# Optimization experiments

Measured on AMD Instinct MI355X. Metric: run time of the kernel, lower is better.

The kernel has to match this reference:

```python
import math
import jax, jax.numpy as jnp
import numpy as np

B, T, C = 2, 2048, 1024
N_HEAD, N_KV_HEAD = 16, 4
HEAD_DIM = C // N_HEAD  # 64

def _rope(x, cos, sin):
    # x: (B, T, H, D); cos/sin: (1, T, 1, D//2)
    d = x.shape[3] // 2
    x1, x2 = x[..., :d], x[..., d:]
    return jnp.concatenate([x1 * cos + x2 * sin, -x1 * sin + x2 * cos], axis=3)

def _rms_norm(x):
    return x * jax.lax.rsqrt(jnp.mean(x * x, axis=-1, keepdims=True) + 1e-06)

def setup_inputs() -> dict:
    key = jax.random.key(0)
    ks = jax.random.split(key, 9)
    x = jax.random.normal(ks[0], (B, T, C), dtype=jnp.float32)
    ve = jax.random.normal(ks[1], (B, T, N_KV_HEAD * HEAD_DIM), dtype=jnp.float32)
    cos = jax.random.uniform(ks[2], (1, T, 1, HEAD_DIM // 2), dtype=jnp.float32)
    sin = jax.random.uniform(ks[3], (1, T, 1, HEAD_DIM // 2), dtype=jnp.float32)
    s = 1.0 / math.sqrt(C)
    Wq = jax.random.normal(ks[4], (C, N_HEAD * HEAD_DIM), dtype=jnp.float32) * s
    Wk = jax.random.normal(ks[5], (C, N_KV_HEAD * HEAD_DIM), dtype=jnp.float32) * s
    Wv = jax.random.normal(ks[6], (C, N_KV_HEAD * HEAD_DIM), dtype=jnp.float32) * s
    Wproj = jax.random.normal(ks[7], (C, C), dtype=jnp.float32) * s
    Wg = jax.random.normal(ks[8], (12, N_KV_HEAD), dtype=jnp.float32) * (1.0 / math.sqrt(12))
    return {"x": x, "ve": ve, "cos": cos, "sin": sin,
            "Wq": Wq, "Wk": Wk, "Wv": Wv, "Wproj": Wproj, "Wg": Wg,
            "window_size": 1024}

def reference(x, ve, cos, sin, Wq, Wk, Wv, Wproj, Wg, window_size):
    Bb, Tt, Cc = x.shape
    q = (x @ Wq).reshape(Bb, Tt, N_HEAD, HEAD_DIM)
    k = (x @ Wk).reshape(Bb, Tt, N_KV_HEAD, HEAD_DIM)
    v = (x @ Wv).reshape(Bb, Tt, N_KV_HEAD, HEAD_DIM)
    # value-embedding gate (has_ve layer)
    vee = ve.reshape(Bb, Tt, N_KV_HEAD, HEAD_DIM)
    gate = 3.0 * jax.nn.sigmoid(x[..., :12] @ Wg)  # (B, T, n_kv_head)
    v = v + gate[..., None] * vee
    q = _rope(q, cos, sin)
    k = _rope(k, cos, sin)
    q = _rms_norm(q) * 1.2
    k = _rms_norm(k) * 1.2
    repeats = N_HEAD // N_KV_HEAD
    k = jnp.repeat(k, repeats, axis=2)
    v = jnp.repeat(v, repeats, axis=2)
    # sliding-window causal mask
    row = jnp.arange(Tt)[:, None]
    col = jnp.arange(Tt)[None, :]
    mask = (row >= col) & (row - col <= window_size)
    bias = jnp.where(mask, 0.0, -1e9)  # (T, T)
    scale = 1.0 / math.sqrt(HEAD_DIM)
    scores = jnp.einsum("bqhd,bkhd->bhqk", q, k) * scale + bias[None, None]
    attn = jax.nn.softmax(scores, axis=-1)
    y = jnp.einsum("bhqk,bkhd->bqhd", attn, v).reshape(Bb, Tt, Cc)
    return y @ Wproj
```

## Files before the change

kernel.cpp:

```cpp
#include <hip/hip_runtime.h>


typedef __bf16 bf16x8 __attribute__((ext_vector_type(8)));
typedef __bf16 bf16x4 __attribute__((ext_vector_type(4)));
typedef float  f32x4  __attribute__((ext_vector_type(4)));

__device__ __forceinline__ void g2l16(const __bf16* gp, __bf16* lp) {
  __builtin_amdgcn_global_load_lds(
      (const __attribute__((address_space(1))) unsigned int*)(const void*)gp,
      (__attribute__((address_space(3))) unsigned int*)(void*)lp, 16, 0, 0);
}

__global__ void prep(const float* __restrict__ x, __bf16* __restrict__ xb,
                     float* __restrict__ gate, const float* __restrict__ Wg,
                     const float* __restrict__ Wq, const float* __restrict__ Wk,
                     const float* __restrict__ Wv, const float* __restrict__ Wp,
                     __bf16* __restrict__ Wt, __bf16* __restrict__ Wpt) {
  __shared__ float tile[32][33];
  int bid = blockIdx.x;
  if (bid < 2048) {
    int i = (bid * 256 + threadIdx.x) * 8;
    float4 a = *(const float4*)(x + i);
    float4 b = *(const float4*)(x + i + 4);
    bf16x8 o;
    o[0] = (__bf16)a.x; o[1] = (__bf16)a.y; o[2] = (__bf16)a.z; o[3] = (__bf16)a.w;
    o[4] = (__bf16)b.x; o[5] = (__bf16)b.y; o[6] = (__bf16)b.z; o[7] = (__bf16)b.w;
    *(bf16x8*)(xb + i) = o;
    if (threadIdx.x < 8) {
      int row = bid * 2 + (threadIdx.x >> 2);
      int kvh = threadIdx.x & 3;
      float dot = 0.f;
      for (int j = 0; j < 12; ++j) dot += x[(size_t)row * 1024 + j] * Wg[j * 4 + kvh];
      gate[row * 4 + kvh] = 3.f / (1.f + expf(-dot));
    }
    return;
  }
  bid -= 2048;
  int z = bid >> 10, r = bid & 1023;
  int bx = r & 31, by = r >> 5;
  const float* in; __bf16* out; int Cc;
  if (z == 0)      { in = Wq; out = Wt;               Cc = 1024; }
  else if (z == 1) { in = Wk; out = Wt + 1024 * 1024; Cc = 256; }
  else if (z == 2) { in = Wv; out = Wt + 1280 * 1024; Cc = 256; }
  else             { in = Wp; out = Wpt;              Cc = 1024; }
  int c0 = bx * 32, r0 = by * 32;
  if (c0 >= Cc) return;
  int tx = threadIdx.x & 31, ty = threadIdx.x >> 5;
  for (int i = ty; i < 32; i += 8) tile[i][tx] = in[(size_t)(r0 + i) * Cc + c0 + tx];
  __syncthreads();
  for (int i = ty; i < 32; i += 8) out[(size_t)(c0 + i) * 1024 + r0 + tx] = (__bf16)tile[tx][i];
}

__global__ __launch_bounds__(256) void gemm_qkv(const __bf16* __restrict__ A,
                                                const __bf16* __restrict__ Bt,
                                                const float* __restrict__ cosp,
                                                const float* __restrict__ sinp,
                                                const float* __restrict__ gate,
                                                const float* __restrict__ ve,
                                                __bf16* __restrict__ Qb,
                                                __bf16* __restrict__ Kb,
                                                __bf16* __restrict__ Vt) {
  const int K = 1024;
  __shared__ __bf16 As[128 * 64];
  __shared__ __bf16 Bs[128 * 64];
  int tid = threadIdx.x;
  int m0 = blockIdx.y * 128, n0 = blockIdx.x * 128;
  int w = tid >> 6, lane = tid & 63, quad = lane >> 4, l16 = lane & 15;
  int wm = (w >> 1) * 64, wn = (w & 1) * 64;

  f32x4 zero = {0.f, 0.f, 0.f, 0.f};
  f32x4 acc[4][4];
  for (int i = 0; i < 4; ++i) for (int j = 0; j < 4; ++j) acc[i][j] = zero;

  int rsub = lane >> 2, cc = (lane & 3) * 8;
  const __bf16* gA0 = A  + (size_t)(m0 + (2 * w) * 16 + rsub) * K + cc;
  const __bf16* gA1 = A  + (size_t)(m0 + (2 * w + 1) * 16 + rsub) * K + cc;
  const __bf16* gB0 = Bt + (size_t)(n0 + (2 * w) * 16 + rsub) * K + cc;
  const __bf16* gB1 = Bt + (size_t)(n0 + (2 * w + 1) * 16 + rsub) * K + cc;
  __bf16* lA00 = &As[(2 * w) * 512];     __bf16* lA01 = &As[4096 + (2 * w) * 512];
  __bf16* lA10 = &As[(2 * w + 1) * 512]; __bf16* lA11 = &As[4096 + (2 * w + 1) * 512];
  __bf16* lB00 = &Bs[(2 * w) * 512];     __bf16* lB01 = &Bs[4096 + (2 * w) * 512];
  __bf16* lB10 = &Bs[(2 * w + 1) * 512]; __bf16* lB11 = &Bs[4096 + (2 * w + 1) * 512];

  for (int k0 = 0; k0 < K; k0 += 64) {
    __syncthreads();
    g2l16(gA0 + k0, lA00); g2l16(gA0 + k0 + 32, lA01);
    g2l16(gA1 + k0, lA10); g2l16(gA1 + k0 + 32, lA11);
    g2l16(gB0 + k0, lB00); g2l16(gB0 + k0 + 32, lB01);
    g2l16(gB1 + k0, lB10); g2l16(gB1 + k0 + 32, lB11);
    __syncthreads();
    for (int ks = 0; ks < 2; ++ks) {
      bf16x8 af[4], bfr[4];
      for (int i = 0; i < 4; ++i) {
        af[i]  = *(const bf16x8*)(&As[ks * 4096 + (wm + i * 16 + l16) * 32 + quad * 8]);
        bfr[i] = *(const bf16x8*)(&Bs[ks * 4096 + (wn + i * 16 + l16) * 32 + quad * 8]);
      }
      for (int i = 0; i < 4; ++i)
        for (int j = 0; j < 4; ++j)
          acc[i][j] = __builtin_amdgcn_mfma_f32_16x16x32_bf16(af[i], bfr[j], acc[i][j], 0, 0, 0);
    }
  }

  int ncol = n0 + wn;
  if (ncol < 1280) {
    __bf16* dstbase;
    if (ncol < 1024) dstbase = Qb + (size_t)(ncol >> 6) * 2048 * 64;
    else             dstbase = Kb + (size_t)((ncol - 1024) >> 6) * 2048 * 64;
    int nheads = (ncol < 1024) ? 16 : 4;
    for (int i = 0; i < 4; ++i) {
      for (int r = 0; r < 4; ++r) {
        int m = m0 + wm + i * 16 + quad * 4 + r;
        int bb = m >> 11, t = m & 2047;
        float c0 = cosp[t * 32 + l16], c1 = cosp[t * 32 + 16 + l16];
        float s0 = sinp[t * 32 + l16], s1 = sinp[t * 32 + 16 + l16];
        float v0 = acc[i][0][r], v1 = acc[i][1][r], v2 = acc[i][2][r], v3 = acc[i][3][r];
        float r0 = v0 * c0 + v2 * s0;
        float r1 = v1 * c1 + v3 * s1;
        float r2 = v2 * c0 - v0 * s0;
        float r3 = v3 * c1 - v1 * s1;
        float ss = r0 * r0 + r1 * r1 + r2 * r2 + r3 * r3;
        ss += __shfl_xor(ss, 1, 64); ss += __shfl_xor(ss, 2, 64);
        ss += __shfl_xor(ss, 4, 64); ss += __shfl_xor(ss, 8, 64);
        float sc = rsqrtf(ss * (1.f / 64.f) + 1e-6f) * 1.2f;
        __bf16* dst = dstbase + ((size_t)bb * nheads * 2048 + t) * 64;
        dst[l16]      = (__bf16)(r0 * sc);
        dst[16 + l16] = (__bf16)(r1 * sc);
        dst[32 + l16] = (__bf16)(r2 * sc);
        dst[48 + l16] = (__bf16)(r3 * sc);
      }
    }
  } else {
    int kvh = (ncol - 1280) >> 6;
    for (int i = 0; i < 4; ++i) {
      int mbase = m0 + wm + i * 16 + quad * 4;
      int bb = mbase >> 11;
      int t0 = mbase & 2047;
      float g4[4];
      for (int r = 0; r < 4; ++r) g4[r] = gate[(mbase + r) * 4 + kvh];
      for (int j = 0; j < 4; ++j) {
        int d = j * 16 + l16;
        bf16x4 pk;
        for (int r = 0; r < 4; ++r)
          pk[r] = (__bf16)(acc[i][j][r] + g4[r] * ve[(size_t)(mbase + r) * 256 + kvh * 64 + d]);
        *(bf16x4*)(Vt + ((size_t)(bb * 4 + kvh) * 64 + d) * 2048 + t0) = pk;
      }
    }
  }
}

__global__ __launch_bounds__(512) void attn_kernel(
    const __bf16* __restrict__ Q, const __bf16* __restrict__ K,
    const __bf16* __restrict__ Vt, __bf16* __restrict__ Y,
    const int* __restrict__ winp) {
  const int T = 2048, D = 64, NH = 16, NKV = 4;
  int b = blockIdx.z, h = blockIdx.y;
  int qb = (15 - blockIdx.x) * 128;
  int kvh = h >> 2;
  int tid = threadIdx.x, w = tid >> 6, lane = tid & 63, quad = lane >> 4, l16 = lane & 15;
  int window = *winp;
  int qw = qb + w * 16;

  __shared__ __bf16 Ks[64 * 72];
  __shared__ __bf16 Vs[64 * 72];

  const __bf16* Qbase = Q + ((size_t)(b * NH + h)) * T * D;
  bf16x8 qf0 = *(const bf16x8*)(Qbase + (size_t)(qw + l16) * D + quad * 8);
  bf16x8 qf1 = *(const bf16x8*)(Qbase + (size_t)(qw + l16) * D + quad * 8 + 32);

  const __bf16* Kbase = K  + ((size_t)(b * NKV + kvh)) * T * D;
  const __bf16* Vbase = Vt + ((size_t)(b * NKV + kvh)) * D * T;

  float lsum = 0.f;
  f32x4 zero = {0.f, 0.f, 0.f, 0.f};
  f32x4 o[4] = {zero, zero, zero, zero};

  int kw = qb - window;
  int kstart = (kw > 0) ? (kw & ~63) : 0;
  int kend = qb + 128;
  const float c1 = 0.125f * 1.44269504f;
  const float c2 = 12.0f * 1.44269504f;
  int q = qw + l16;

  int sr = tid >> 3, sc8 = (tid & 7) * 8;
  bf16x8 kr = *(const bf16x8*)(Kbase + (size_t)(kstart + sr) * D + sc8);
  bf16x8 vr = *(const bf16x8*)(Vbase + (size_t)sr * T + kstart + sc8);

  for (int kt = kstart; kt < kend; kt += 64) {
    __syncthreads();
    *(bf16x8*)(&Ks[sr * 72 + sc8]) = kr;
    *(bf16x8*)(&Vs[sr * 72 + sc8]) = vr;
    __syncthreads();
    int ktn = kt + 64;
    if (ktn < kend) {
      kr = *(const bf16x8*)(Kbase + (size_t)(ktn + sr) * D + sc8);
      vr = *(const bf16x8*)(Vbase + (size_t)sr * T + ktn + sc8);
    }
    if (kt > qw + 15 || kt + 63 < qw - window) continue;
    bool clean = (kt + 63 <= qw) && (qw + 15 - kt <= window);

    for (int g = 0; g < 2; ++g) {
      int kb = g * 32;
      bf16x8 ka0 = *(const bf16x8*)(&Ks[(kb + l16) * 72 + quad * 8]);
      bf16x8 ka1 = *(const bf16x8*)(&Ks[(kb + l16) * 72 + quad * 8 + 32]);
      f32x4 sA = __builtin_amdgcn_mfma_f32_16x16x32_bf16(ka0, qf0, zero, 0, 0, 0);
      sA       = __builtin_amdgcn_mfma_f32_16x16x32_bf16(ka1, qf1, sA, 0, 0, 0);
      bf16x8 kb0 = *(const bf16x8*)(&Ks[(kb + 16 + l16) * 72 + quad * 8]);
      bf16x8 kb1 = *(const bf16x8*)(&Ks[(kb + 16 + l16) * 72 + quad * 8 + 32]);
      f32x4 sB = __builtin_amdgcn_mfma_f32_16x16x32_bf16(kb0, qf0, zero, 0, 0, 0);
      sB       = __builtin_amdgcn_mfma_f32_16x16x32_bf16(kb1, qf1, sB, 0, 0, 0);

      bf16x8 pf;
      if (clean) {
        for (int r = 0; r < 4; ++r) {
          float pA = __builtin_amdgcn_exp2f(sA[r] * c1 - c2);
          float pB = __builtin_amdgcn_exp2f(sB[r] * c1 - c2);
          lsum += pA + pB;
          pf[r] = (__bf16)pA; pf[4 + r] = (__bf16)pB;
        }
      } else {
        for (int r = 0; r < 4; ++r) {
          int kiA = kt + kb + quad * 4 + r;
          int kiB = kiA + 16;
          bool okA = (kiA <= q) && (q - kiA <= window);
          bool okB = (kiB <= q) && (q - kiB <= window);
          float pA = okA ? __builtin_amdgcn_exp2f(sA[r] * c1 - c2) : 0.f;
          float pB = okB ? __builtin_amdgcn_exp2f(sB[r] * c1 - c2) : 0.f;
          lsum += pA + pB;
          pf[r] = (__bf16)pA; pf[4 + r] = (__bf16)pB;
        }
      }
      for (int dc = 0; dc < 4; ++dc) {
        bf16x4 va = *(const bf16x4*)(&Vs[(dc * 16 + l16) * 72 + kb + quad * 4]);
        bf16x4 vb = *(const bf16x4*)(&Vs[(dc * 16 + l16) * 72 + kb + 16 + quad * 4]);
        bf16x8 vf;
        vf[0] = va[0]; vf[1] = va[1]; vf[2] = va[2]; vf[3] = va[3];
        vf[4] = vb[0]; vf[5] = vb[1]; vf[6] = vb[2]; vf[7] = vb[3];
        o[dc] = __builtin_amdgcn_mfma_f32_16x16x32_bf16(vf, pf, o[dc], 0, 0, 0);
      }
    }
  }

  float l = lsum;
  l += __shfl_xor(l, 16, 64);
  l += __shfl_xor(l, 32, 64);
  float inv = 1.f / l;
  size_t base = ((size_t)(b * T + q)) * 1024 + h * 64 + quad * 4;
  for (int dc = 0; dc < 4; ++dc) {
    bf16x4 pk;
    pk[0] = (__bf16)(o[dc][0] * inv); pk[1] = (__bf16)(o[dc][1] * inv);
    pk[2] = (__bf16)(o[dc][2] * inv); pk[3] = (__bf16)(o[dc][3] * inv);
    *(bf16x4*)(Y + base + dc * 16) = pk;
  }
}

__global__ __launch_bounds__(256) void gemm_proj(const __bf16* __restrict__ A,
                                                 const __bf16* __restrict__ Bt,
                                                 float* __restrict__ C,
                                                 int M, int N, int K) {
  __shared__ __bf16 As[128 * 64];
  __shared__ __bf16 Bs[128 * 64];
  int tid = threadIdx.x;
  int m0 = blockIdx.y * 128, n0 = blockIdx.x * 128;
  int w = tid >> 6, lane = tid & 63, quad = lane >> 4, l16 = lane & 15;
  int wm = (w >> 1) * 64, wn = (w & 1) * 64;

  f32x4 zero = {0.f, 0.f, 0.f, 0.f};
  f32x4 acc[4][4];
  for (int i = 0; i < 4; ++i) for (int j = 0; j < 4; ++j) acc[i][j] = zero;

  int rsub = lane >> 2, cc = (lane & 3) * 8;
  const __bf16* gA0 = A  + (size_t)(m0 + (2 * w) * 16 + rsub) * K + cc;
  const __bf16* gA1 = A  + (size_t)(m0 + (2 * w + 1) * 16 + rsub) * K + cc;
  const __bf16* gB0 = Bt + (size_t)(n0 + (2 * w) * 16 + rsub) * K + cc;
  const __bf16* gB1 = Bt + (size_t)(n0 + (2 * w + 1) * 16 + rsub) * K + cc;
  __bf16* lA00 = &As[(2 * w) * 512];     __bf16* lA01 = &As[4096 + (2 * w) * 512];
  __bf16* lA10 = &As[(2 * w + 1) * 512]; __bf16* lA11 = &As[4096 + (2 * w + 1) * 512];
  __bf16* lB00 = &Bs[(2 * w) * 512];     __bf16* lB01 = &Bs[4096 + (2 * w) * 512];
  __bf16* lB10 = &Bs[(2 * w + 1) * 512]; __bf16* lB11 = &Bs[4096 + (2 * w + 1) * 512];

  for (int k0 = 0; k0 < K; k0 += 64) {
    __syncthreads();
    g2l16(gA0 + k0, lA00); g2l16(gA0 + k0 + 32, lA01);
    g2l16(gA1 + k0, lA10); g2l16(gA1 + k0 + 32, lA11);
    g2l16(gB0 + k0, lB00); g2l16(gB0 + k0 + 32, lB01);
    g2l16(gB1 + k0, lB10); g2l16(gB1 + k0 + 32, lB11);
    __syncthreads();
    for (int ks = 0; ks < 2; ++ks) {
      bf16x8 af[4], bfr[4];
      for (int i = 0; i < 4; ++i) {
        af[i]  = *(const bf16x8*)(&As[ks * 4096 + (wm + i * 16 + l16) * 32 + quad * 8]);
        bfr[i] = *(const bf16x8*)(&Bs[ks * 4096 + (wn + i * 16 + l16) * 32 + quad * 8]);
      }
      for (int i = 0; i < 4; ++i)
        for (int j = 0; j < 4; ++j)
          acc[i][j] = __builtin_amdgcn_mfma_f32_16x16x32_bf16(af[i], bfr[j], acc[i][j], 0, 0, 0);
    }
  }
  for (int i = 0; i < 4; ++i)
    for (int j = 0; j < 4; ++j)
      for (int r = 0; r < 4; ++r)
        C[(size_t)(m0 + wm + i * 16 + quad * 4 + r) * N + n0 + wn + j * 16 + l16] = acc[i][j][r];
}

extern "C" void kernel_launch(void* const* d_in, const int* in_sizes, int n_in,
                              void* d_out, int out_size, void* d_ws, size_t ws_size,
                              hipStream_t stream) {
  const float* x     = (const float*)d_in[0];
  const float* ve    = (const float*)d_in[1];
  const float* cosp  = (const float*)d_in[2];
  const float* sinp  = (const float*)d_in[3];
  const float* Wq    = (const float*)d_in[4];
  const float* Wk    = (const float*)d_in[5];
  const float* Wv    = (const float*)d_in[6];
  const float* Wproj = (const float*)d_in[7];
  const float* Wg    = (const float*)d_in[8];
  const int*   win   = (const int*)d_in[9];
  float* out = (float*)d_out;

  char* ws = (char*)d_ws;
  __bf16* xb   = (__bf16*)(ws);
  __bf16* Wt   = (__bf16*)(ws + 8388608);
  __bf16* Wpt  = (__bf16*)(ws + 11534336);
  float*  gate = (float*)(ws + 13631488);
  __bf16* Qb   = (__bf16*)(ws + 13697024);
  __bf16* Kb   = (__bf16*)(ws + 22085632);
  __bf16* Vt   = (__bf16*)(ws + 24182784);
  __bf16* Y    = (__bf16*)(ws + 26279936);

  prep<<<2048 + 4096, 256, 0, stream>>>(x, xb, gate, Wg, Wq, Wk, Wv, Wproj, Wt, Wpt);
  gemm_qkv<<<dim3(12, 32), 256, 0, stream>>>(xb, Wt, cosp, sinp, gate, ve, Qb, Kb, Vt);
  attn_kernel<<<dim3(16, 16, 2), 512, 0, stream>>>(Qb, Kb, Vt, Y, win);
  gemm_proj<<<dim3(8, 32), 256, 0, stream>>>(Y, Wpt, out, 4096, 1024, 1024);
}
```

Baseline: 178.9 us.

## Halve GEMM M-tile for more blocks and remap attention blocks for KV locality

```diff
diff --git a/kernel.cpp b/kernel.cpp
--- a/kernel.cpp
+++ b/kernel.cpp
@@ -61,41 +61,38 @@
                                                 __bf16* __restrict__ Kb,
                                                 __bf16* __restrict__ Vt) {
   const int K = 1024;
-  __shared__ __bf16 As[128 * 64];
-  __shared__ __bf16 Bs[128 * 64];
+  __shared__ __bf16 As[2 * 64 * 32];
+  __shared__ __bf16 Bs[2 * 128 * 32];
   int tid = threadIdx.x;
-  int m0 = blockIdx.y * 128, n0 = blockIdx.x * 128;
+  int m0 = blockIdx.y * 64, n0 = blockIdx.x * 128;
   int w = tid >> 6, lane = tid & 63, quad = lane >> 4, l16 = lane & 15;
-  int wm = (w >> 1) * 64, wn = (w & 1) * 64;
+  int wm = (w >> 1) * 32, wn = (w & 1) * 64;
 
   f32x4 zero = {0.f, 0.f, 0.f, 0.f};
-  f32x4 acc[4][4];
-  for (int i = 0; i < 4; ++i) for (int j = 0; j < 4; ++j) acc[i][j] = zero;
+  f32x4 acc[2][4];
+  for (int i = 0; i < 2; ++i) for (int j = 0; j < 4; ++j) acc[i][j] = zero;
 
   int rsub = lane >> 2, cc = (lane & 3) * 8;
-  const __bf16* gA0 = A  + (size_t)(m0 + (2 * w) * 16 + rsub) * K + cc;
-  const __bf16* gA1 = A  + (size_t)(m0 + (2 * w + 1) * 16 + rsub) * K + cc;
+  const __bf16* gA  = A  + (size_t)(m0 + w * 16 + rsub) * K + cc;
   const __bf16* gB0 = Bt + (size_t)(n0 + (2 * w) * 16 + rsub) * K + cc;
   const __bf16* gB1 = Bt + (size_t)(n0 + (2 * w + 1) * 16 + rsub) * K + cc;
-  __bf16* lA00 = &As[(2 * w) * 512];     __bf16* lA01 = &As[4096 + (2 * w) * 512];
-  __bf16* lA10 = &As[(2 * w + 1) * 512]; __bf16* lA11 = &As[4096 + (2 * w + 1) * 512];
-  __bf16* lB00 = &Bs[(2 * w) * 512];     __bf16* lB01 = &Bs[4096 + (2 * w) * 512];
-  __bf16* lB10 = &Bs[(2 * w + 1) * 512]; __bf16* lB11 = &Bs[4096 + (2 * w + 1) * 512];
+  __bf16* lA0  = &As[w * 512];            __bf16* lA1  = &As[2048 + w * 512];
+  __bf16* lB00 = &Bs[(2 * w) * 512];      __bf16* lB01 = &Bs[4096 + (2 * w) * 512];
+  __bf16* lB10 = &Bs[(2 * w + 1) * 512];  __bf16* lB11 = &Bs[4096 + (2 * w + 1) * 512];
 
   for (int k0 = 0; k0 < K; k0 += 64) {
     __syncthreads();
-    g2l16(gA0 + k0, lA00); g2l16(gA0 + k0 + 32, lA01);
-    g2l16(gA1 + k0, lA10); g2l16(gA1 + k0 + 32, lA11);
-    g2l16(gB0 + k0, lB00); g2l16(gB0 + k0 + 32, lB01);
-    g2l16(gB1 + k0, lB10); g2l16(gB1 + k0 + 32, lB11);
+    g2l16(gA + k0, lA0);       g2l16(gA + k0 + 32, lA1);
+    g2l16(gB0 + k0, lB00);     g2l16(gB0 + k0 + 32, lB01);
+    g2l16(gB1 + k0, lB10);     g2l16(gB1 + k0 + 32, lB11);
     __syncthreads();
     for (int ks = 0; ks < 2; ++ks) {
-      bf16x8 af[4], bfr[4];
-      for (int i = 0; i < 4; ++i) {
-        af[i]  = *(const bf16x8*)(&As[ks * 4096 + (wm + i * 16 + l16) * 32 + quad * 8]);
-        bfr[i] = *(const bf16x8*)(&Bs[ks * 4096 + (wn + i * 16 + l16) * 32 + quad * 8]);
-      }
-      for (int i = 0; i < 4; ++i)
+      bf16x8 af[2], bfr[4];
+      for (int i = 0; i < 2; ++i)
+        af[i] = *(const bf16x8*)(&As[ks * 2048 + (wm + i * 16 + l16) * 32 + quad * 8]);
+      for (int j = 0; j < 4; ++j)
+        bfr[j] = *(const bf16x8*)(&Bs[ks * 4096 + (wn + j * 16 + l16) * 32 + quad * 8]);
+      for (int i = 0; i < 2; ++i)
         for (int j = 0; j < 4; ++j)
           acc[i][j] = __builtin_amdgcn_mfma_f32_16x16x32_bf16(af[i], bfr[j], acc[i][j], 0, 0, 0);
     }
@@ -107,7 +104,7 @@
     if (ncol < 1024) dstbase = Qb + (size_t)(ncol >> 6) * 2048 * 64;
     else             dstbase = Kb + (size_t)((ncol - 1024) >> 6) * 2048 * 64;
     int nheads = (ncol < 1024) ? 16 : 4;
-    for (int i = 0; i < 4; ++i) {
+    for (int i = 0; i < 2; ++i) {
       for (int r = 0; r < 4; ++r) {
         int m = m0 + wm + i * 16 + quad * 4 + r;
         int bb = m >> 11, t = m & 2047;
@@ -131,7 +128,7 @@
     }
   } else {
     int kvh = (ncol - 1280) >> 6;
-    for (int i = 0; i < 4; ++i) {
+    for (int i = 0; i < 2; ++i) {
       int mbase = m0 + wm + i * 16 + quad * 4;
       int bb = mbase >> 11;
       int t0 = mbase & 2047;
@@ -153,9 +150,11 @@
     const __bf16* __restrict__ Vt, __bf16* __restrict__ Y,
     const int* __restrict__ winp) {
   const int T = 2048, D = 64, NH = 16, NKV = 4;
-  int b = blockIdx.z, h = blockIdx.y;
-  int qb = (15 - blockIdx.x) * 128;
-  int kvh = h >> 2;
+  int fid = blockIdx.x + 16 * blockIdx.y + 256 * blockIdx.z;
+  int g8 = fid & 7, j = fid >> 3;
+  int b = g8 >> 2, kvh = g8 & 3;
+  int h = kvh * 4 + (j & 3);
+  int qb = (15 - (j >> 2)) * 128;
   int tid = threadIdx.x, w = tid >> 6, lane = tid & 63, quad = lane >> 4, l16 = lane & 15;
   int window = *winp;
   int qw = qb + w * 16;
@@ -257,46 +256,43 @@
                                                  const __bf16* __restrict__ Bt,
                                                  float* __restrict__ C,
                                                  int M, int N, int K) {
-  __shared__ __bf16 As[128 * 64];
-  __shared__ __bf16 Bs[128 * 64];
+  __shared__ __bf16 As[2 * 64 * 32];
+  __shared__ __bf16 Bs[2 * 128 * 32];
   int tid = threadIdx.x;
-  int m0 = blockIdx.y * 128, n0 = blockIdx.x * 128;
+  int m0 = blockIdx.y * 64, n0 = blockIdx.x * 128;
   int w = tid >> 6, lane = tid & 63, quad = lane >> 4, l16 = lane & 15;
-  int wm = (w >> 1) * 64, wn = (w & 1) * 64;
+  int wm = (w >> 1) * 32, wn = (w & 1) * 64;
 
   f32x4 zero = {0.f, 0.f, 0.f, 0.f};
-  f32x4 acc[4][4];
-  for (int i = 0; i < 4; ++i) for (int j = 0; j < 4; ++j) acc[i][j] = zero;
+  f32x4 acc[2][4];
+  for (int i = 0; i < 2; ++i) for (int j = 0; j < 4; ++j) acc[i][j] = zero;
 
   int rsub = lane >> 2, cc = (lane & 3) * 8;
-  const __bf16* gA0 = A  + (size_t)(m0 + (2 * w) * 16 + rsub) * K + cc;
-  const __bf16* gA1 = A  + (size_t)(m0 + (2 * w + 1) * 16 + rsub) * K + cc;
+  const __bf16* gA  = A  + (size_t)(m0 + w * 16 + rsub) * K + cc;
   const __bf16* gB0 = Bt + (size_t)(n0 + (2 * w) * 16 + rsub) * K + cc;
   const __bf16* gB1 = Bt + (size_t)(n0 + (2 * w + 1) * 16 + rsub) * K + cc;
-  __bf16* lA00 = &As[(2 * w) * 512];     __bf16* lA01 = &As[4096 + (2 * w) * 512];
-  __bf16* lA10 = &As[(2 * w + 1) * 512]; __bf16* lA11 = &As[4096 + (2 * w + 1) * 512];
-  __bf16* lB00 = &Bs[(2 * w) * 512];     __bf16* lB01 = &Bs[4096 + (2 * w) * 512];
-  __bf16* lB10 = &Bs[(2 * w + 1) * 512]; __bf16* lB11 = &Bs[4096 + (2 * w + 1) * 512];
+  __bf16* lA0  = &As[w * 512];            __bf16* lA1  = &As[2048 + w * 512];
+  __bf16* lB00 = &Bs[(2 * w) * 512];      __bf16* lB01 = &Bs[4096 + (2 * w) * 512];
+  __bf16* lB10 = &Bs[(2 * w + 1) * 512];  __bf16* lB11 = &Bs[4096 + (2 * w + 1) * 512];
 
   for (int k0 = 0; k0 < K; k0 += 64) {
     __syncthreads();
-    g2l16(gA0 + k0, lA00); g2l16(gA0 + k0 + 32, lA01);
-    g2l16(gA1 + k0, lA10); g2l16(gA1 + k0 + 32, lA11);
-    g2l16(gB0 + k0, lB00); g2l16(gB0 + k0 + 32, lB01);
-    g2l16(gB1 + k0, lB10); g2l16(gB1 + k0 + 32, lB11);
+    g2l16(gA + k0, lA0);       g2l16(gA + k0 + 32, lA1);
+    g2l16(gB0 + k0, lB00);     g2l16(gB0 + k0 + 32, lB01);
+    g2l16(gB1 + k0, lB10);     g2l16(gB1 + k0 + 32, lB11);
     __syncthreads();
     for (int ks = 0; ks < 2; ++ks) {
-      bf16x8 af[4], bfr[4];
-      for (int i = 0; i < 4; ++i) {
-        af[i]  = *(const bf16x8*)(&As[ks * 4096 + (wm + i * 16 + l16) * 32 + quad * 8]);
-        bfr[i] = *(const bf16x8*)(&Bs[ks * 4096 + (wn + i * 16 + l16) * 32 + quad * 8]);
-      }
-      for (int i = 0; i < 4; ++i)
+      bf16x8 af[2], bfr[4];
+      for (int i = 0; i < 2; ++i)
+        af[i] = *(const bf16x8*)(&As[ks * 2048 + (wm + i * 16 + l16) * 32 + quad * 8]);
+      for (int j = 0; j < 4; ++j)
+        bfr[j] = *(const bf16x8*)(&Bs[ks * 4096 + (wn + j * 16 + l16) * 32 + quad * 8]);
+      for (int i = 0; i < 2; ++i)
         for (int j = 0; j < 4; ++j)
           acc[i][j] = __builtin_amdgcn_mfma_f32_16x16x32_bf16(af[i], bfr[j], acc[i][j], 0, 0, 0);
     }
   }
-  for (int i = 0; i < 4; ++i)
+  for (int i = 0; i < 2; ++i)
     for (int j = 0; j < 4; ++j)
       for (int r = 0; r < 4; ++r)
         C[(size_t)(m0 + wm + i * 16 + quad * 4 + r) * N + n0 + wn + j * 16 + l16] = acc[i][j][r];
@@ -328,7 +324,7 @@
   __bf16* Y    = (__bf16*)(ws + 26279936);
 
   prep<<<2048 + 4096, 256, 0, stream>>>(x, xb, gate, Wg, Wq, Wk, Wv, Wproj, Wt, Wpt);
-  gemm_qkv<<<dim3(12, 32), 256, 0, stream>>>(xb, Wt, cosp, sinp, gate, ve, Qb, Kb, Vt);
+  gemm_qkv<<<dim3(12, 64), 256, 0, stream>>>(xb, Wt, cosp, sinp, gate, ve, Qb, Kb, Vt);
   attn_kernel<<<dim3(16, 16, 2), 512, 0, stream>>>(Qb, Kb, Vt, Y, win);
-  gemm_proj<<<dim3(8, 32), 256, 0, stream>>>(Y, Wpt, out, 4096, 1024, 1024);
-}
+  gemm_proj<<<dim3(8, 64), 256, 0, stream>>>(Y, Wpt, out, 4096, 1024, 1024);
+}
```

Result: faster. 167.4 us (-6.4%).

## Use single-wave 64x64 double-buffered GEMMs and group attention blocks by KV head

Applied to the files above, without the earlier changes.

```diff
diff --git a/kernel.cpp b/kernel.cpp
--- a/kernel.cpp
+++ b/kernel.cpp
@@ -51,57 +51,59 @@
   for (int i = ty; i < 32; i += 8) out[(size_t)(c0 + i) * 1024 + r0 + tx] = (__bf16)tile[tx][i];
 }
 
-__global__ __launch_bounds__(256) void gemm_qkv(const __bf16* __restrict__ A,
-                                                const __bf16* __restrict__ Bt,
-                                                const float* __restrict__ cosp,
-                                                const float* __restrict__ sinp,
-                                                const float* __restrict__ gate,
-                                                const float* __restrict__ ve,
-                                                __bf16* __restrict__ Qb,
-                                                __bf16* __restrict__ Kb,
-                                                __bf16* __restrict__ Vt) {
+__global__ __launch_bounds__(64, 2) void gemm_qkv(const __bf16* __restrict__ A,
+                                                  const __bf16* __restrict__ Bt,
+                                                  const float* __restrict__ cosp,
+                                                  const float* __restrict__ sinp,
+                                                  const float* __restrict__ gate,
+                                                  const float* __restrict__ ve,
+                                                  __bf16* __restrict__ Qb,
+                                                  __bf16* __restrict__ Kb,
+                                                  __bf16* __restrict__ Vt) {
   const int K = 1024;
-  __shared__ __bf16 As[128 * 64];
-  __shared__ __bf16 Bs[128 * 64];
-  int tid = threadIdx.x;
-  int m0 = blockIdx.y * 128, n0 = blockIdx.x * 128;
-  int w = tid >> 6, lane = tid & 63, quad = lane >> 4, l16 = lane & 15;
-  int wm = (w >> 1) * 64, wn = (w & 1) * 64;
+  __shared__ __bf16 As[2][64 * 32];
+  __shared__ __bf16 Bs[2][64 * 32];
+  int lane = threadIdx.x, quad = lane >> 4, l16 = lane & 15;
+  int m0 = blockIdx.y * 64, n0 = blockIdx.x * 64;
 
   f32x4 zero = {0.f, 0.f, 0.f, 0.f};
   f32x4 acc[4][4];
   for (int i = 0; i < 4; ++i) for (int j = 0; j < 4; ++j) acc[i][j] = zero;
 
   int rsub = lane >> 2, cc = (lane & 3) * 8;
-  const __bf16* gA0 = A  + (size_t)(m0 + (2 * w) * 16 + rsub) * K + cc;
-  const __bf16* gA1 = A  + (size_t)(m0 + (2 * w + 1) * 16 + rsub) * K + cc;
-  const __bf16* gB0 = Bt + (size_t)(n0 + (2 * w) * 16 + rsub) * K + cc;
-  const __bf16* gB1 = Bt + (size_t)(n0 + (2 * w + 1) * 16 + rsub) * K + cc;
-  __bf16* lA00 = &As[(2 * w) * 512];     __bf16* lA01 = &As[4096 + (2 * w) * 512];
-  __bf16* lA10 = &As[(2 * w + 1) * 512]; __bf16* lA11 = &As[4096 + (2 * w + 1) * 512];
-  __bf16* lB00 = &Bs[(2 * w) * 512];     __bf16* lB01 = &Bs[4096 + (2 * w) * 512];
-  __bf16* lB10 = &Bs[(2 * w + 1) * 512]; __bf16* lB11 = &Bs[4096 + (2 * w + 1) * 512];
-
-  for (int k0 = 0; k0 < K; k0 += 64) {
-    __syncthreads();
-    g2l16(gA0 + k0, lA00); g2l16(gA0 + k0 + 32, lA01);
-    g2l16(gA1 + k0, lA10); g2l16(gA1 + k0 + 32, lA11);
-    g2l16(gB0 + k0, lB00); g2l16(gB0 + k0 + 32, lB01);
-    g2l16(gB1 + k0, lB10); g2l16(gB1 + k0 + 32, lB11);
-    __syncthreads();
-    for (int ks = 0; ks < 2; ++ks) {
-      bf16x8 af[4], bfr[4];
-      for (int i = 0; i < 4; ++i) {
-        af[i]  = *(const bf16x8*)(&As[ks * 4096 + (wm + i * 16 + l16) * 32 + quad * 8]);
-        bfr[i] = *(const bf16x8*)(&Bs[ks * 4096 + (wn + i * 16 + l16) * 32 + quad * 8]);
-      }
-      for (int i = 0; i < 4; ++i)
-        for (int j = 0; j < 4; ++j)
-          acc[i][j] = __builtin_amdgcn_mfma_f32_16x16x32_bf16(af[i], bfr[j], acc[i][j], 0, 0, 0);
-    }
-  }
-
-  int ncol = n0 + wn;
+  const __bf16* gA = A  + (size_t)(m0 + rsub) * K + cc;
+  const __bf16* gB = Bt + (size_t)(n0 + rsub) * K + cc;
+
+  for (int c = 0; c < 4; ++c) {
+    g2l16(gA + c * 16 * K, &As[0][c * 512]);
+    g2l16(gB + c * 16 * K, &Bs[0][c * 512]);
+  }
+  for (int it = 0; it < 32; ++it) {
+    int cur = it & 1;
+    if (it + 1 < 32) {
+      int k1 = (it + 1) * 32;
+      for (int c = 0; c < 4; ++c) {
+        g2l16(gA + c * 16 * K + k1, &As[cur ^ 1][c * 512]);
+        g2l16(gB + c * 16 * K + k1, &Bs[cur ^ 1][c * 512]);
+      }
+      __builtin_amdgcn_sched_barrier(0);
+      __builtin_amdgcn_s_waitcnt(0xF78);
+    } else {
+      __builtin_amdgcn_sched_barrier(0);
+      __builtin_amdgcn_s_waitcnt(0xF70);
+    }
+    __builtin_amdgcn_sched_barrier(0);
+    bf16x8 af[4], bfr[4];
+    for (int i = 0; i < 4; ++i) {
+      af[i]  = *(const bf16x8*)(&As[cur][(i * 16 + l16) * 32 + quad * 8]);
+      bfr[i] = *(const bf16x8*)(&Bs[cur][(i * 16 + l16) * 32 + quad * 8]);
+    }
+    for (int i = 0; i < 4; ++i)
+      for (int j = 0; j < 4; ++j)
+        acc[i][j] = __builtin_amdgcn_mfma_f32_16x16x32_bf16(af[i], bfr[j], acc[i][j], 0, 0, 0);
+  }
+
+  int ncol = n0;
   if (ncol < 1280) {
     __bf16* dstbase;
     if (ncol < 1024) dstbase = Qb + (size_t)(ncol >> 6) * 2048 * 64;
@@ -109,7 +111,7 @@
     int nheads = (ncol < 1024) ? 16 : 4;
     for (int i = 0; i < 4; ++i) {
       for (int r = 0; r < 4; ++r) {
-        int m = m0 + wm + i * 16 + quad * 4 + r;
+        int m = m0 + i * 16 + quad * 4 + r;
         int bb = m >> 11, t = m & 2047;
         float c0 = cosp[t * 32 + l16], c1 = cosp[t * 32 + 16 + l16];
         float s0 = sinp[t * 32 + l16], s1 = sinp[t * 32 + 16 + l16];
@@ -132,7 +134,7 @@
   } else {
     int kvh = (ncol - 1280) >> 6;
     for (int i = 0; i < 4; ++i) {
-      int mbase = m0 + wm + i * 16 + quad * 4;
+      int mbase = m0 + i * 16 + quad * 4;
       int bb = mbase >> 11;
       int t0 = mbase & 2047;
       float g4[4];
@@ -153,9 +155,11 @@
     const __bf16* __restrict__ Vt, __bf16* __restrict__ Y,
     const int* __restrict__ winp) {
   const int T = 2048, D = 64, NH = 16, NKV = 4;
-  int b = blockIdx.z, h = blockIdx.y;
-  int qb = (15 - blockIdx.x) * 128;
-  int kvh = h >> 2;
+  int fid = blockIdx.x + 16 * blockIdx.y + 256 * blockIdx.z;
+  int g8 = fid & 7, j = fid >> 3;
+  int b = g8 >> 2, kvh = g8 & 3;
+  int h = kvh * 4 + (j & 3);
+  int qb = (15 - (j >> 2)) * 128;
   int tid = threadIdx.x, w = tid >> 6, lane = tid & 63, quad = lane >> 4, l16 = lane & 15;
   int window = *winp;
   int qw = qb + w * 16;
@@ -253,53 +257,56 @@
   }
 }
 
-__global__ __launch_bounds__(256) void gemm_proj(const __bf16* __restrict__ A,
-                                                 const __bf16* __restrict__ Bt,
-                                                 float* __restrict__ C,
-                                                 int M, int N, int K) {
-  __shared__ __bf16 As[128 * 64];
-  __shared__ __bf16 Bs[128 * 64];
-  int tid = threadIdx.x;
-  int m0 = blockIdx.y * 128, n0 = blockIdx.x * 128;
-  int w = tid >> 6, lane = tid & 63, quad = lane >> 4, l16 = lane & 15;
-  int wm = (w >> 1) * 64, wn = (w & 1) * 64;
+__global__ __launch_bounds__(64, 2) void gemm_proj(const __bf16* __restrict__ A,
+                                                   const __bf16* __restrict__ Bt,
+                                                   float* __restrict__ C,
+                                                   int M, int N, int K) {
+  __shared__ __bf16 As[2][64 * 32];
+  __shared__ __bf16 Bs[2][64 * 32];
+  int lane = threadIdx.x, quad = lane >> 4, l16 = lane & 15;
+  int m0 = blockIdx.y * 64, n0 = blockIdx.x * 64;
 
   f32x4 zero = {0.f, 0.f, 0.f, 0.f};
   f32x4 acc[4][4];
   for (int i = 0; i < 4; ++i) for (int j = 0; j < 4; ++j) acc[i][j] = zero;
 
   int rsub = lane >> 2, cc = (lane & 3) * 8;
-  const __bf16* gA0 = A  + (size_t)(m0 + (2 * w) * 16 + rsub) * K + cc;
-  const __bf16* gA1 = A  + (size_t)(m0 + (2 * w + 1) * 16 + rsub) * K + cc;
-  const __bf16* gB0 = Bt + (size_t)(n0 + (2 * w) * 16 + rsub) * K + cc;
-  const __bf16* gB1 = Bt + (size_t)(n0 + (2 * w + 1) * 16 + rsub) * K + cc;
-  __bf16* lA00 = &As[(2 * w) * 512];     __bf16* lA01 = &As[4096 + (2 * w) * 512];
-  __bf16* lA10 = &As[(2 * w + 1) * 512]; __bf16* lA11 = &As[4096 + (2 * w + 1) * 512];
-  __bf16* lB00 = &Bs[(2 * w) * 512];     __bf16* lB01 = &Bs[4096 + (2 * w) * 512];
-  __bf16* lB10 = &Bs[(2 * w + 1) * 512]; __bf16* lB11 = &Bs[4096 + (2 * w + 1) * 512];
-
-  for (int k0 = 0; k0 < K; k0 += 64) {
-    __syncthreads();
-    g2l16(gA0 + k0, lA00); g2l16(gA0 + k0 + 32, lA01);
-    g2l16(gA1 + k0, lA10); g2l16(gA1 + k0 + 32, lA11);
-    g2l16(gB0 + k0, lB00); g2l16(gB0 + k0 + 32, lB01);
-    g2l16(gB1 + k0, lB10); g2l16(gB1 + k0 + 32, lB11);
-    __syncthreads();
-    for (int ks = 0; ks < 2; ++ks) {
-      bf16x8 af[4], bfr[4];
-      for (int i = 0; i < 4; ++i) {
-        af[i]  = *(const bf16x8*)(&As[ks * 4096 + (wm + i * 16 + l16) * 32 + quad * 8]);
-        bfr[i] = *(const bf16x8*)(&Bs[ks * 4096 + (wn + i * 16 + l16) * 32 + quad * 8]);
-      }
-      for (int i = 0; i < 4; ++i)
-        for (int j = 0; j < 4; ++j)
-          acc[i][j] = __builtin_amdgcn_mfma_f32_16x16x32_bf16(af[i], bfr[j], acc[i][j], 0, 0, 0);
-    }
+  const __bf16* gA = A  + (size_t)(m0 + rsub) * K + cc;
+  const __bf16* gB = Bt + (size_t)(n0 + rsub) * K + cc;
+
+  for (int c = 0; c < 4; ++c) {
+    g2l16(gA + c * 16 * K, &As[0][c * 512]);
+    g2l16(gB + c * 16 * K, &Bs[0][c * 512]);
+  }
+  int iters = K / 32;
+  for (int it = 0; it < iters; ++it) {
+    int cur = it & 1;
+    if (it + 1 < iters) {
+      int k1 = (it + 1) * 32;
+      for (int c = 0; c < 4; ++c) {
+        g2l16(gA + c * 16 * K + k1, &As[cur ^ 1][c * 512]);
+        g2l16(gB + c * 16 * K + k1, &Bs[cur ^ 1][c * 512]);
+      }
+      __builtin_amdgcn_sched_barrier(0);
+      __builtin_amdgcn_s_waitcnt(0xF78);
+    } else {
+      __builtin_amdgcn_sched_barrier(0);
+      __builtin_amdgcn_s_waitcnt(0xF70);
+    }
+    __builtin_amdgcn_sched_barrier(0);
+    bf16x8 af[4], bfr[4];
+    for (int i = 0; i < 4; ++i) {
+      af[i]  = *(const bf16x8*)(&As[cur][(i * 16 + l16) * 32 + quad * 8]);
+      bfr[i] = *(const bf16x8*)(&Bs[cur][(i * 16 + l16) * 32 + quad * 8]);
+    }
+    for (int i = 0; i < 4; ++i)
+      for (int j = 0; j < 4; ++j)
+        acc[i][j] = __builtin_amdgcn_mfma_f32_16x16x32_bf16(af[i], bfr[j], acc[i][j], 0, 0, 0);
   }
   for (int i = 0; i < 4; ++i)
     for (int j = 0; j < 4; ++j)
       for (int r = 0; r < 4; ++r)
-        C[(size_t)(m0 + wm + i * 16 + quad * 4 + r) * N + n0 + wn + j * 16 + l16] = acc[i][j][r];
+        C[(size_t)(m0 + i * 16 + quad * 4 + r) * N + n0 + j * 16 + l16] = acc[i][j][r];
 }
 
 extern "C" void kernel_launch(void* const* d_in, const int* in_sizes, int n_in,
@@ -328,7 +335,7 @@
   __bf16* Y    = (__bf16*)(ws + 26279936);
 
   prep<<<2048 + 4096, 256, 0, stream>>>(x, xb, gate, Wg, Wq, Wk, Wv, Wproj, Wt, Wpt);
-  gemm_qkv<<<dim3(12, 32), 256, 0, stream>>>(xb, Wt, cosp, sinp, gate, ve, Qb, Kb, Vt);
+  gemm_qkv<<<dim3(24, 64), 64, 0, stream>>>(xb, Wt, cosp, sinp, gate, ve, Qb, Kb, Vt);
   attn_kernel<<<dim3(16, 16, 2), 512, 0, stream>>>(Qb, Kb, Vt, Y, win);
-  gemm_proj<<<dim3(8, 32), 256, 0, stream>>>(Y, Wpt, out, 4096, 1024, 1024);
-}
+  gemm_proj<<<dim3(16, 64), 64, 0, stream>>>(Y, Wpt, out, 4096, 1024, 1024);
+}
```

Result: no change. 176.1 us (-1.6%).
